# Performance work log

Hardware: AMD Instinct MI355X
Metric: run time of the kernel (lower is better)

Reference implementation:

```python
import jax, jax.numpy as jnp
import numpy as np


def setup_inputs() -> dict:
    key = jax.random.key(0)
    kq, kc = jax.random.split(key)
    query = jax.random.normal(kq, (64, 768), dtype=jnp.float32)
    corpus = jax.random.normal(kc, (500000, 768), dtype=jnp.float32)
    return {"query": query, "corpus": corpus, "k": 16}


def reference(query, corpus, k):
    # cosine similarity: (q @ c.T) / (|q|[:,None] * |c|[None,:])  -> [B, N]
    sim = jnp.einsum("bd,nd->bn", query, corpus)
    qn = jnp.linalg.norm(query, axis=1)   # [B]
    cn = jnp.linalg.norm(corpus, axis=1)  # [N]
    sim = sim / (qn[:, None] * cn[None, :])
    # top-k most similar corpus entries per query (largest=True)
    values, indices = jax.lax.top_k(sim, k)  # [B, k], [B, k]
    return values, indices
```

## Files before the change

### kernel.cpp

```cpp
#include <hip/hip_runtime.h>
#include <hip/hip_bf16.h>

#define D 768
#define NQ 64
#define TPB 256
#define GRID 1303
#define NWAVES (GRID * 4)
#define KSTEPS 24
#define SIMP 20
#define NS 8

typedef float    f32x4 __attribute__((ext_vector_type(4)));
typedef _Float16 h16x8 __attribute__((ext_vector_type(8)));

__device__ __forceinline__ bool kbetter(float v1, int i1, float v2, int i2) {
    return (v1 > v2) || (v1 == v2 && i1 < i2);
}

__device__ __forceinline__ void topk_insert(float (&tv)[16], int (&ti)[16], float v, int idx) {
    if (!kbetter(v, idx, tv[15], ti[15])) return;
    tv[15] = v; ti[15] = idx;
    #pragma unroll
    for (int s = 15; s >= 1; --s) {
        bool sw = kbetter(tv[s], ti[s], tv[s-1], ti[s-1]);
        float av = sw ? tv[s] : tv[s-1];
        float bv = sw ? tv[s-1] : tv[s];
        int   ai = sw ? ti[s] : ti[s-1];
        int   bi = sw ? ti[s-1] : ti[s];
        tv[s-1] = av; tv[s] = bv; ti[s-1] = ai; ti[s] = bi;
    }
}

__device__ __forceinline__ void bitonic16(float (&v)[16], int (&ix)[16]) {
    #pragma unroll
    for (int d = 8; d >= 1; d >>= 1) {
        #pragma unroll
        for (int i = 0; i < 16; ++i) {
            if ((i & d) == 0) {
                int j = i | d;
                bool sw = kbetter(v[j], ix[j], v[i], ix[i]);
                float av = sw ? v[j] : v[i];
                float bv = sw ? v[i] : v[j];
                int   ai = sw ? ix[j] : ix[i];
                int   bi = sw ? ix[i] : ix[j];
                v[i] = av; v[j] = bv; ix[i] = ai; ix[j] = bi;
            }
        }
    }
}

__device__ __forceinline__ void lane_merge(float (&v)[16], int (&ix)[16], int mask) {
    float pv[16]; int pix[16];
    #pragma unroll
    for (int i = 0; i < 16; ++i) {
        pv[i]  = __shfl_xor(v[15 - i], mask);
        pix[i] = __shfl_xor(ix[15 - i], mask);
    }
    #pragma unroll
    for (int i = 0; i < 16; ++i) {
        if (kbetter(pv[i], pix[i], v[i], ix[i])) { v[i] = pv[i]; ix[i] = pix[i]; }
    }
    bitonic16(v, ix);
}

__device__ __forceinline__ void sort64(float& v, int& ix, int l) {
    #pragma unroll
    for (int k = 2; k <= 64; k <<= 1) {
        #pragma unroll
        for (int j = k >> 1; j >= 1; j >>= 1) {
            float ov = __shfl_xor(v, j);
            int   oi = __shfl_xor(ix, j);
            bool dirDesc = ((l & k) == 0);
            bool lower   = ((l & j) == 0);
            bool takeBetter = (lower == dirDesc);
            bool ob = kbetter(ov, oi, v, ix);
            if (takeBetter == ob) { v = ov; ix = oi; }
        }
    }
}

__global__ __launch_bounds__(256)
void prep_kernel(const float* __restrict__ query, _Float16* __restrict__ qpk) {
    int b = blockIdx.x, t = threadIdx.x;
    const float* row = query + b * D;
    float vals[3]; float s = 0.f;
    #pragma unroll
    for (int j = 0; j < 3; ++j) { vals[j] = row[t + 256 * j]; s += vals[j] * vals[j]; }
    #pragma unroll
    for (int m = 1; m < 64; m <<= 1) s += __shfl_xor(s, m);
    __shared__ float ws4[4];
    if ((t & 63) == 0) ws4[t >> 6] = s;
    __syncthreads();
    float qn = sqrtf(ws4[0] + ws4[1] + ws4[2] + ws4[3]);
    int qf = b >> 4;
    #pragma unroll
    for (int j = 0; j < 3; ++j) {
        int col = t + 256 * j;
        float vn = vals[j] / qn;
        _Float16 h = (_Float16)vn;
        float r = vn - (float)h;
        _Float16 l2 = (_Float16)(r * 2048.0f);
        int ks = col >> 5, unit = (col >> 3) & 3, sub = col & 7;
        int lane = (b & 15) + unit * 16;
        size_t off = (((size_t)ks * 4 + qf) * 64 + lane) * 16 + sub;
        qpk[off]     = h;
        qpk[off + 8] = l2;
    }
}

__global__ __launch_bounds__(TPB, 2)
void sim_topk_kernel(const float* __restrict__ corpus,
                     const _Float16* __restrict__ qpk,
                     float2* __restrict__ cand,
                     int N, int NG) {
    __shared__ float scratch[4][NQ * SIMP];
    int t = threadIdx.x, w = t >> 6, l = t & 63;
    int ww = blockIdx.x * 4 + w;
    int n16 = l & 15, kg = l >> 4;
    float* sc = scratch[w];

    float tv[16]; int ti[16];
    #pragma unroll
    for (int s = 0; s < 16; ++s) { tv[s] = -INFINITY; ti[s] = 0x7fffffff; }

    for (int g = ww; g < NG; g += NWAVES) {
        long baseA = (long)g * 32;
        long rA = baseA + n16;      if (rA > N - 1) rA = N - 1;
        long rB = baseA + 16 + n16; if (rB > N - 1) rB = N - 1;
        const float* pA = corpus + (size_t)rA * D + kg * 8;
        const float* pB = corpus + (size_t)rB * D + kg * 8;

        f32x4 accAH[4], accAX[4], accBH[4], accBX[4];
        #pragma unroll
        for (int qf = 0; qf < 4; ++qf) {
            accAH[qf] = (f32x4)(0.f); accAX[qf] = (f32x4)(0.f);
            accBH[qf] = (f32x4)(0.f); accBX[qf] = (f32x4)(0.f);
        }
        float psA = 0.f, psB = 0.f;

        #pragma unroll 2
        for (int ks = 0; ks < KSTEPS; ++ks) {
            h16x8 qh[4], ql[4];
            #pragma unroll
            for (int qf = 0; qf < 4; ++qf) {
                const _Float16* qp = qpk + (((size_t)ks * 4 + qf) * 64 + l) * 16;
                qh[qf] = *(const h16x8*)qp;
                ql[qf] = *(const h16x8*)(qp + 8);
            }
            f32x4 a0 = *(const f32x4*)(pA + ks * 32);
            f32x4 a1 = *(const f32x4*)(pA + ks * 32 + 4);
            f32x4 b0 = *(const f32x4*)(pB + ks * 32);
            f32x4 b1 = *(const f32x4*)(pB + ks * 32 + 4);

            h16x8 hiA, loA, hiB, loB;
            #pragma unroll
            for (int i = 0; i < 4; ++i) {
                float va = a0[i]; _Float16 ha = (_Float16)va;
                hiA[i] = ha; loA[i] = (_Float16)((va - (float)ha) * 2048.0f);
                psA += va * va;
                float va1 = a1[i]; _Float16 ha1 = (_Float16)va1;
                hiA[4 + i] = ha1; loA[4 + i] = (_Float16)((va1 - (float)ha1) * 2048.0f);
                psA += va1 * va1;
                float vb = b0[i]; _Float16 hb = (_Float16)vb;
                hiB[i] = hb; loB[i] = (_Float16)((vb - (float)hb) * 2048.0f);
                psB += vb * vb;
                float vb1 = b1[i]; _Float16 hb1 = (_Float16)vb1;
                hiB[4 + i] = hb1; loB[4 + i] = (_Float16)((vb1 - (float)hb1) * 2048.0f);
                psB += vb1 * vb1;
            }
            #pragma unroll
            for (int qf = 0; qf < 4; ++qf) {
                accAH[qf] = __builtin_amdgcn_mfma_f32_16x16x32_f16(qh[qf], hiA, accAH[qf], 0, 0, 0);
                accAX[qf] = __builtin_amdgcn_mfma_f32_16x16x32_f16(qh[qf], loA, accAX[qf], 0, 0, 0);
                accAX[qf] = __builtin_amdgcn_mfma_f32_16x16x32_f16(ql[qf], hiA, accAX[qf], 0, 0, 0);
                accBH[qf] = __builtin_amdgcn_mfma_f32_16x16x32_f16(qh[qf], hiB, accBH[qf], 0, 0, 0);
                accBX[qf] = __builtin_amdgcn_mfma_f32_16x16x32_f16(qh[qf], loB, accBX[qf], 0, 0, 0);
                accBX[qf] = __builtin_amdgcn_mfma_f32_16x16x32_f16(ql[qf], hiB, accBX[qf], 0, 0, 0);
            }
        }

        psA += __shfl_xor(psA, 16); psA += __shfl_xor(psA, 32);
        psB += __shfl_xor(psB, 16); psB += __shfl_xor(psB, 32);
        float invA = 1.0f / sqrtf(psA);
        float invB = 1.0f / sqrtf(psB);

        #pragma unroll
        for (int qf = 0; qf < 4; ++qf)
            #pragma unroll
            for (int r = 0; r < 4; ++r) {
                int q = qf * 16 + kg * 4 + r;
                sc[q * SIMP + n16] = (accAH[qf][r] + accAX[qf][r] * (1.0f / 2048.0f)) * invA;
            }
        {
            f32x4 sv[4];
            #pragma unroll
            for (int j = 0; j < 4; ++j) sv[j] = *(const f32x4*)(sc + l * SIMP + j * 4);
            #pragma unroll
            for (int j = 0; j < 4; ++j)
                #pragma unroll
                for (int e = 0; e < 4; ++e) {
                    long gidx = baseA + j * 4 + e;
                    if (gidx < N) topk_insert(tv, ti, sv[j][e], (int)gidx);
                }
        }
        #pragma unroll
        for (int qf = 0; qf < 4; ++qf)
            #pragma unroll
            for (int r = 0; r < 4; ++r) {
                int q = qf * 16 + kg * 4 + r;
                sc[q * SIMP + n16] = (accBH[qf][r] + accBX[qf][r] * (1.0f / 2048.0f)) * invB;
            }
        {
            f32x4 sv[4];
            #pragma unroll
            for (int j = 0; j < 4; ++j) sv[j] = *(const f32x4*)(sc + l * SIMP + j * 4);
            #pragma unroll
            for (int j = 0; j < 4; ++j)
                #pragma unroll
                for (int e = 0; e < 4; ++e) {
                    long gidx = baseA + 16 + j * 4 + e;
                    if (gidx < N) topk_insert(tv, ti, sv[j][e], (int)gidx);
                }
        }
    }

    float2* dst = cand + ((size_t)l * NWAVES + ww) * 16;
    #pragma unroll
    for (int s = 0; s < 16; ++s) dst[s] = make_float2(tv[s], __int_as_float(ti[s]));
}

__global__ __launch_bounds__(256)
void merge1_kernel(const float2* __restrict__ cand, float2* __restrict__ cand2, int NWV) {
    int q = blockIdx.x >> 3, seg = blockIdx.x & (NS - 1);
    int t = threadIdx.x, w = t >> 6, l = t & 63;
    int total = NWV * 16;
    int chunk = (total + NS - 1) / NS;
    int e0 = seg * chunk, e1 = min(total, e0 + chunk);
    const float2* src = cand + (size_t)q * total;
    float tv[16]; int ti[16];
    #pragma unroll
    for (int s = 0; s < 16; ++s) { tv[s] = -INFINITY; ti[s] = 0x7fffffff; }
    for (int e = e0 + t; e < e1; e += 256) {
        float2 ce = src[e];
        topk_insert(tv, ti, ce.x, __float_as_int(ce.y));
    }
    lane_merge(tv, ti, 1);  lane_merge(tv, ti, 2);  lane_merge(tv, ti, 4);
    lane_merge(tv, ti, 8);  lane_merge(tv, ti, 16); lane_merge(tv, ti, 32);
    __shared__ float2 stage[64];
    if (l == 0) {
        #pragma unroll
        for (int s = 0; s < 16; ++s) stage[w * 16 + s] = make_float2(tv[s], __int_as_float(ti[s]));
    }
    __syncthreads();
    if (t < 64) {
        float2 ce = stage[t];
        float v = ce.x; int ix = __float_as_int(ce.y);
        sort64(v, ix, t);
        if (t < 16) cand2[((size_t)q * NS + seg) * 16 + t] = make_float2(v, __int_as_float(ix));
    }
}

__global__ __launch_bounds__(64)
void merge2_kernel(const float2* __restrict__ cand2, float* __restrict__ out) {
    int q = blockIdx.x, l = threadIdx.x;
    const float2* src = cand2 + (size_t)q * (NS * 16);
    float2 a = src[l], b = src[l + 64];
    float v1 = a.x; int i1 = __float_as_int(a.y);
    float v2 = b.x; int i2 = __float_as_int(b.y);
    sort64(v1, i1, l);
    sort64(v2, i2, l);
    float sv = __shfl(v2, (l - 16) & 63);
    int   si = __shfl(i2, (l - 16) & 63);
    float mv = (l < 16) ? v1 : ((l < 32) ? sv : -INFINITY);
    int   mi = (l < 16) ? i1 : ((l < 32) ? si : 0x7fffffff);
    sort64(mv, mi, l);
    if (l < 16) {
        out[q * 16 + l]           = mv;
        out[NQ * 16 + q * 16 + l] = (float)mi;
    }
}

extern "C" void kernel_launch(void* const* d_in, const int* in_sizes, int n_in,
                              void* d_out, int out_size, void* d_ws, size_t ws_size,
                              hipStream_t stream) {
    const float* query  = (const float*)d_in[0];
    const float* corpus = (const float*)d_in[1];
    int N  = in_sizes[1] / D;
    int NG = (N + 31) / 32;
    char* ws = (char*)d_ws;
    _Float16* qpk = (_Float16*)ws;
    float2*  cand = (float2*)(ws + 196608);
    size_t candBytes = (size_t)NQ * NWAVES * 16 * sizeof(float2);
    float2* cand2 = (float2*)(ws + 196608 + candBytes);
    float*   out  = (float*)d_out;

    prep_kernel<<<NQ, 256, 0, stream>>>(query, qpk);
    sim_topk_kernel<<<GRID, TPB, 0, stream>>>(corpus, qpk, cand, N, NG);
    merge1_kernel<<<NQ * NS, 256, 0, stream>>>(cand, cand2, NWAVES);
    merge2_kernel<<<NQ, 64, 0, stream>>>(cand2, out);
}
```

Before: 614.2 us.

## Split query and corpus rows across waves with software-pipelined loads

Each wave now computes 16 corpus rows against 32 queries, not 32 rows against all 64 queries, so the four waves of a block split a 32-row group by row half and query half. Accumulator registers drop sharply, launch bounds rise to 4 blocks per CU, and the k-loop is fully unrolled with double-buffered corpus and query loads for the next step. Lanes 0-31 and 32-63 hold separate top-k lists for the same query, so they are merged with lane_merge and only half the lanes write candidates. Fewer candidates go to the merge stage, but each corpus row is now converted and norm-summed by two waves, which duplicates that ALU and load work.

```diff
diff --git a/kernel.cpp b/kernel.cpp
--- a/kernel.cpp
+++ b/kernel.cpp
@@ -4,10 +4,10 @@
 #define D 768
 #define NQ 64
 #define TPB 256
-#define GRID 1303
-#define NWAVES (GRID * 4)
+#define GRID 1024
+#define NPAIR (GRID * 2)
 #define KSTEPS 24
-#define SIMP 20
+#define SCST 17
 #define NS 8
 
 typedef float    f32x4 __attribute__((ext_vector_type(4)));
@@ -108,14 +108,52 @@
     }
 }
 
-__global__ __launch_bounds__(TPB, 2)
+
+#define QLOADM(ks, qh0, ql0, qh1, ql1) do {                                    \
+    const _Float16* qp0 = qpk + (((size_t)(ks) * 4 + qb) * 64 + l) * 16;       \
+    qh0 = *(const h16x8*)qp0;  ql0 = *(const h16x8*)(qp0 + 8);                 \
+    const _Float16* qp1 = qp0 + 64 * 16;                                       \
+    qh1 = *(const h16x8*)qp1;  ql1 = *(const h16x8*)(qp1 + 8);                 \
+  } while (0)
+
+#define CLOADM(ks, c0, c1) do {                                                \
+    c0 = *(const f32x4*)(pc + (ks) * 32);                                      \
+    c1 = *(const f32x4*)(pc + (ks) * 32 + 4);                                  \
+  } while (0)
+
+#define STEPM(ks, c0, c1, qh0, ql0, qh1, ql1, n0, n1, nqh0, nql0, nqh1, nql1)  \
+  do {                                                                         \
+    if ((ks) + 1 < KSTEPS) {                                                   \
+        CLOADM((ks) + 1, n0, n1);                                              \
+        QLOADM((ks) + 1, nqh0, nql0, nqh1, nql1);                              \
+    }                                                                          \
+    h16x8 hi, lo;                                                              \
+    _Pragma("unroll")                                                          \
+    for (int i = 0; i < 4; ++i) {                                              \
+        float v0 = c0[i]; _Float16 h0 = (_Float16)v0;                          \
+        hi[i] = h0; lo[i] = (_Float16)((v0 - (float)h0) * 2048.0f);            \
+        ps += v0 * v0;                                                         \
+        float v1 = c1[i]; _Float16 h1 = (_Float16)v1;                          \
+        hi[4 + i] = h1; lo[4 + i] = (_Float16)((v1 - (float)h1) * 2048.0f);    \
+        ps += v1 * v1;                                                         \
+    }                                                                          \
+    aH0 = __builtin_amdgcn_mfma_f32_16x16x32_f16(qh0, hi, aH0, 0, 0, 0);       \
+    aX0 = __builtin_amdgcn_mfma_f32_16x16x32_f16(qh0, lo, aX0, 0, 0, 0);       \
+    aX0 = __builtin_amdgcn_mfma_f32_16x16x32_f16(ql0, hi, aX0, 0, 0, 0);       \
+    aH1 = __builtin_amdgcn_mfma_f32_16x16x32_f16(qh1, hi, aH1, 0, 0, 0);       \
+    aX1 = __builtin_amdgcn_mfma_f32_16x16x32_f16(qh1, lo, aX1, 0, 0, 0);       \
+    aX1 = __builtin_amdgcn_mfma_f32_16x16x32_f16(ql1, hi, aX1, 0, 0, 0);       \
+  } while (0)
+
+__global__ __launch_bounds__(TPB, 4)
 void sim_topk_kernel(const float* __restrict__ corpus,
                      const _Float16* __restrict__ qpk,
                      float2* __restrict__ cand,
                      int N, int NG) {
-    __shared__ float scratch[4][NQ * SIMP];
+    __shared__ float scratch[4][32 * SCST];
     int t = threadIdx.x, w = t >> 6, l = t & 63;
-    int ww = blockIdx.x * 4 + w;
+    int h  = w >> 1;
+    int qb = (w & 1) * 2;
     int n16 = l & 15, kg = l >> 4;
     float* sc = scratch[w];
 
@@ -123,110 +161,67 @@
     #pragma unroll
     for (int s = 0; s < 16; ++s) { tv[s] = -INFINITY; ti[s] = 0x7fffffff; }
 
-    for (int g = ww; g < NG; g += NWAVES) {
-        long baseA = (long)g * 32;
-        long rA = baseA + n16;      if (rA > N - 1) rA = N - 1;
-        long rB = baseA + 16 + n16; if (rB > N - 1) rB = N - 1;
-        const float* pA = corpus + (size_t)rA * D + kg * 8;
-        const float* pB = corpus + (size_t)rB * D + kg * 8;
-
-        f32x4 accAH[4], accAX[4], accBH[4], accBX[4];
-        #pragma unroll
-        for (int qf = 0; qf < 4; ++qf) {
-            accAH[qf] = (f32x4)(0.f); accAX[qf] = (f32x4)(0.f);
-            accBH[qf] = (f32x4)(0.f); accBX[qf] = (f32x4)(0.f);
-        }
-        float psA = 0.f, psB = 0.f;
-
-        #pragma unroll 2
-        for (int ks = 0; ks < KSTEPS; ++ks) {
-            h16x8 qh[4], ql[4];
-            #pragma unroll
-            for (int qf = 0; qf < 4; ++qf) {
-                const _Float16* qp = qpk + (((size_t)ks * 4 + qf) * 64 + l) * 16;
-                qh[qf] = *(const h16x8*)qp;
-                ql[qf] = *(const h16x8*)(qp + 8);
-            }
-            f32x4 a0 = *(const f32x4*)(pA + ks * 32);
-            f32x4 a1 = *(const f32x4*)(pA + ks * 32 + 4);
-            f32x4 b0 = *(const f32x4*)(pB + ks * 32);
-            f32x4 b1 = *(const f32x4*)(pB + ks * 32 + 4);
-
-            h16x8 hiA, loA, hiB, loB;
-            #pragma unroll
-            for (int i = 0; i < 4; ++i) {
-                float va = a0[i]; _Float16 ha = (_Float16)va;
-                hiA[i] = ha; loA[i] = (_Float16)((va - (float)ha) * 2048.0f);
-                psA += va * va;
-                float va1 = a1[i]; _Float16 ha1 = (_Float16)va1;
-                hiA[4 + i] = ha1; loA[4 + i] = (_Float16)((va1 - (float)ha1) * 2048.0f);
-                psA += va1 * va1;
-                float vb = b0[i]; _Float16 hb = (_Float16)vb;
-                hiB[i] = hb; loB[i] = (_Float16)((vb - (float)hb) * 2048.0f);
-                psB += vb * vb;
-                float vb1 = b1[i]; _Float16 hb1 = (_Float16)vb1;
-                hiB[4 + i] = hb1; loB[4 + i] = (_Float16)((vb1 - (float)hb1) * 2048.0f);
-                psB += vb1 * vb1;
-            }
-            #pragma unroll
-            for (int qf = 0; qf < 4; ++qf) {
-                accAH[qf] = __builtin_amdgcn_mfma_f32_16x16x32_f16(qh[qf], hiA, accAH[qf], 0, 0, 0);
-                accAX[qf] = __builtin_amdgcn_mfma_f32_16x16x32_f16(qh[qf], loA, accAX[qf], 0, 0, 0);
-                accAX[qf] = __builtin_amdgcn_mfma_f32_16x16x32_f16(ql[qf], hiA, accAX[qf], 0, 0, 0);
-                accBH[qf] = __builtin_amdgcn_mfma_f32_16x16x32_f16(qh[qf], hiB, accBH[qf], 0, 0, 0);
-                accBX[qf] = __builtin_amdgcn_mfma_f32_16x16x32_f16(qh[qf], loB, accBX[qf], 0, 0, 0);
-                accBX[qf] = __builtin_amdgcn_mfma_f32_16x16x32_f16(ql[qf], hiB, accBX[qf], 0, 0, 0);
-            }
-        }
-
-        psA += __shfl_xor(psA, 16); psA += __shfl_xor(psA, 32);
-        psB += __shfl_xor(psB, 16); psB += __shfl_xor(psB, 32);
-        float invA = 1.0f / sqrtf(psA);
-        float invB = 1.0f / sqrtf(psB);
-
-        #pragma unroll
-        for (int qf = 0; qf < 4; ++qf)
+    for (int g = blockIdx.x; g < NG; g += GRID) {
+        long rowg = (long)g * 32 + h * 16 + n16;
+        if (rowg > N - 1) rowg = N - 1;
+        const float* pc = corpus + (size_t)rowg * D + kg * 8;
+
+        f32x4 aH0 = (f32x4)(0.f), aX0 = (f32x4)(0.f);
+        f32x4 aH1 = (f32x4)(0.f), aX1 = (f32x4)(0.f);
+        float ps = 0.f;
+
+        f32x4 cA0, cA1, cB0, cB1;
+        h16x8 qhA0, qlA0, qhA1, qlA1, qhB0, qlB0, qhB1, qlB1;
+        CLOADM(0, cA0, cA1);
+        QLOADM(0, qhA0, qlA0, qhA1, qlA1);
+
+        #pragma unroll
+        for (int m = 0; m < KSTEPS / 2; ++m) {
+            STEPM(2 * m,     cA0, cA1, qhA0, qlA0, qhA1, qlA1,
+                             cB0, cB1, qhB0, qlB0, qhB1, qlB1);
+            STEPM(2 * m + 1, cB0, cB1, qhB0, qlB0, qhB1, qlB1,
+                             cA0, cA1, qhA0, qlA0, qhA1, qlA1);
+        }
+
+        ps += __shfl_xor(ps, 16);
+        ps += __shfl_xor(ps, 32);
+        float inv = 1.0f / sqrtf(ps);
+
+        #pragma unroll
+        for (int qf = 0; qf < 2; ++qf)
             #pragma unroll
             for (int r = 0; r < 4; ++r) {
-                int q = qf * 16 + kg * 4 + r;
-                sc[q * SIMP + n16] = (accAH[qf][r] + accAX[qf][r] * (1.0f / 2048.0f)) * invA;
+                int qloc = qf * 16 + kg * 4 + r;
+                float dH = qf ? aH1[r] : aH0[r];
+                float dX = qf ? aX1[r] : aX0[r];
+                sc[qloc * SCST + n16] = (dH + dX * (1.0f / 2048.0f)) * inv;
             }
         {
-            f32x4 sv[4];
+            int qloc = l & 31, nh = (l >> 5) * 8;
+            f32x4 s0 = *(const f32x4*)(sc + qloc * SCST + nh);
+            f32x4 s1 = *(const f32x4*)(sc + qloc * SCST + nh + 4);
+            long gbase = (long)g * 32 + h * 16 + nh;
             #pragma unroll
-            for (int j = 0; j < 4; ++j) sv[j] = *(const f32x4*)(sc + l * SIMP + j * 4);
+            for (int e = 0; e < 4; ++e) {
+                long gi = gbase + e;
+                if (gi < N) topk_insert(tv, ti, s0[e], (int)gi);
+            }
             #pragma unroll
-            for (int j = 0; j < 4; ++j)
-                #pragma unroll
-                for (int e = 0; e < 4; ++e) {
-                    long gidx = baseA + j * 4 + e;
-                    if (gidx < N) topk_insert(tv, ti, sv[j][e], (int)gidx);
-                }
-        }
-        #pragma unroll
-        for (int qf = 0; qf < 4; ++qf)
-            #pragma unroll
-            for (int r = 0; r < 4; ++r) {
-                int q = qf * 16 + kg * 4 + r;
-                sc[q * SIMP + n16] = (accBH[qf][r] + accBX[qf][r] * (1.0f / 2048.0f)) * invB;
-            }
-        {
-            f32x4 sv[4];
-            #pragma unroll
-            for (int j = 0; j < 4; ++j) sv[j] = *(const f32x4*)(sc + l * SIMP + j * 4);
-            #pragma unroll
-            for (int j = 0; j < 4; ++j)
-                #pragma unroll
-                for (int e = 0; e < 4; ++e) {
-                    long gidx = baseA + 16 + j * 4 + e;
-                    if (gidx < N) topk_insert(tv, ti, sv[j][e], (int)gidx);
-                }
-        }
-    }
-
-    float2* dst = cand + ((size_t)l * NWAVES + ww) * 16;
-    #pragma unroll
-    for (int s = 0; s < 16; ++s) dst[s] = make_float2(tv[s], __int_as_float(ti[s]));
+            for (int e = 0; e < 4; ++e) {
+                long gi = gbase + 4 + e;
+                if (gi < N) topk_insert(tv, ti, s1[e], (int)gi);
+            }
+        }
+    }
+
+    lane_merge(tv, ti, 32);
+    if (l < 32) {
+        int q = (w & 1) * 32 + l;
+        int pair = blockIdx.x * 2 + h;
+        float2* dst = cand + ((size_t)q * NPAIR + pair) * 16;
+        #pragma unroll
+        for (int s = 0; s < 16; ++s) dst[s] = make_float2(tv[s], __int_as_float(ti[s]));
+    }
 }
 
 __global__ __launch_bounds__(256)
@@ -290,12 +285,12 @@
     char* ws = (char*)d_ws;
     _Float16* qpk = (_Float16*)ws;
     float2*  cand = (float2*)(ws + 196608);
-    size_t candBytes = (size_t)NQ * NWAVES * 16 * sizeof(float2);
+    size_t candBytes = (size_t)NQ * NPAIR * 16 * sizeof(float2);
     float2* cand2 = (float2*)(ws + 196608 + candBytes);
     float*   out  = (float*)d_out;
 
     prep_kernel<<<NQ, 256, 0, stream>>>(query, qpk);
     sim_topk_kernel<<<GRID, TPB, 0, stream>>>(corpus, qpk, cand, N, NG);
-    merge1_kernel<<<NQ * NS, 256, 0, stream>>>(cand, cand2, NWAVES);
+    merge1_kernel<<<NQ * NS, 256, 0, stream>>>(cand, cand2, NPAIR);
     merge2_kernel<<<NQ, 64, 0, stream>>>(cand2, out);
 }
```

Result: slower. 1.564 ms (+154.6%).

## Split fused similarity+topk into separate sim kernel and streaming top-k merge kernel

Applied to the files above, without the earlier changes.

The fused kernel that computed similarities and kept per-lane top-k in registers is split in two. A leaner sim kernel (one 16-row tile per iteration, fewer registers, occupancy 4) writes the full similarity matrix to workspace with nontemporal stores. A new mergeA kernel streams that matrix and keeps the top-k. This frees MFMA waves from the branchy insertion work and raises occupancy, at the cost of writing and rereading a 128MB similarity buffer.

```diff
diff --git a/kernel.cpp b/kernel.cpp
--- a/kernel.cpp
+++ b/kernel.cpp
@@ -4,10 +4,11 @@
 #define D 768
 #define NQ 64
 #define TPB 256
-#define GRID 1303
-#define NWAVES (GRID * 4)
+#define GRID 1024
+#define NWT (GRID * 4)
 #define KSTEPS 24
-#define SIMP 20
+#define SCST 17
+#define NMW 4096
 #define NS 8
 
 typedef float    f32x4 __attribute__((ext_vector_type(4)));
@@ -108,123 +109,100 @@
     }
 }
 
-__global__ __launch_bounds__(TPB, 2)
-void sim_topk_kernel(const float* __restrict__ corpus,
-                     const _Float16* __restrict__ qpk,
-                     float2* __restrict__ cand,
-                     int N, int NG) {
-    __shared__ float scratch[4][NQ * SIMP];
+__global__ __launch_bounds__(TPB, 4)
+void sim_kernel(const float* __restrict__ corpus,
+                const _Float16* __restrict__ qpk,
+                float* __restrict__ simout, int N, int NG16) {
+    __shared__ float scratch[4][NQ * SCST];
     int t = threadIdx.x, w = t >> 6, l = t & 63;
     int ww = blockIdx.x * 4 + w;
     int n16 = l & 15, kg = l >> 4;
     float* sc = scratch[w];
 
-    float tv[16]; int ti[16];
-    #pragma unroll
-    for (int s = 0; s < 16; ++s) { tv[s] = -INFINITY; ti[s] = 0x7fffffff; }
-
-    for (int g = ww; g < NG; g += NWAVES) {
-        long baseA = (long)g * 32;
-        long rA = baseA + n16;      if (rA > N - 1) rA = N - 1;
-        long rB = baseA + 16 + n16; if (rB > N - 1) rB = N - 1;
-        const float* pA = corpus + (size_t)rA * D + kg * 8;
-        const float* pB = corpus + (size_t)rB * D + kg * 8;
-
-        f32x4 accAH[4], accAX[4], accBH[4], accBX[4];
-        #pragma unroll
-        for (int qf = 0; qf < 4; ++qf) {
-            accAH[qf] = (f32x4)(0.f); accAX[qf] = (f32x4)(0.f);
-            accBH[qf] = (f32x4)(0.f); accBX[qf] = (f32x4)(0.f);
-        }
-        float psA = 0.f, psB = 0.f;
+    for (int g = ww; g < NG16; g += NWT) {
+        long rowg = (long)g * 16 + n16;
+        if (rowg > N - 1) rowg = N - 1;
+        const float* pc = corpus + (size_t)rowg * D + kg * 8;
+
+        f32x4 accH[4], accX[4];
+        #pragma unroll
+        for (int qf = 0; qf < 4; ++qf) { accH[qf] = (f32x4)(0.f); accX[qf] = (f32x4)(0.f); }
+        float ps = 0.f;
 
         #pragma unroll 2
         for (int ks = 0; ks < KSTEPS; ++ks) {
-            h16x8 qh[4], ql[4];
+            f32x4 c0 = __builtin_nontemporal_load((const f32x4*)(pc + ks * 32));
+            f32x4 c1 = __builtin_nontemporal_load((const f32x4*)(pc + ks * 32 + 4));
+            h16x8 hi, lo;
+            #pragma unroll
+            for (int i = 0; i < 4; ++i) {
+                float v0 = c0[i]; _Float16 h0 = (_Float16)v0;
+                hi[i] = h0; lo[i] = (_Float16)((v0 - (float)h0) * 2048.0f);
+                ps += v0 * v0;
+                float v1 = c1[i]; _Float16 h1 = (_Float16)v1;
+                hi[4 + i] = h1; lo[4 + i] = (_Float16)((v1 - (float)h1) * 2048.0f);
+                ps += v1 * v1;
+            }
             #pragma unroll
             for (int qf = 0; qf < 4; ++qf) {
                 const _Float16* qp = qpk + (((size_t)ks * 4 + qf) * 64 + l) * 16;
-                qh[qf] = *(const h16x8*)qp;
-                ql[qf] = *(const h16x8*)(qp + 8);
-            }
-            f32x4 a0 = *(const f32x4*)(pA + ks * 32);
-            f32x4 a1 = *(const f32x4*)(pA + ks * 32 + 4);
-            f32x4 b0 = *(const f32x4*)(pB + ks * 32);
-            f32x4 b1 = *(const f32x4*)(pB + ks * 32 + 4);
-
-            h16x8 hiA, loA, hiB, loB;
-            #pragma unroll
-            for (int i = 0; i < 4; ++i) {
-                float va = a0[i]; _Float16 ha = (_Float16)va;
-                hiA[i] = ha; loA[i] = (_Float16)((va - (float)ha) * 2048.0f);
-                psA += va * va;
-                float va1 = a1[i]; _Float16 ha1 = (_Float16)va1;
-                hiA[4 + i] = ha1; loA[4 + i] = (_Float16)((va1 - (float)ha1) * 2048.0f);
-                psA += va1 * va1;
-                float vb = b0[i]; _Float16 hb = (_Float16)vb;
-                hiB[i] = hb; loB[i] = (_Float16)((vb - (float)hb) * 2048.0f);
-                psB += vb * vb;
-                float vb1 = b1[i]; _Float16 hb1 = (_Float16)vb1;
-                hiB[4 + i] = hb1; loB[4 + i] = (_Float16)((vb1 - (float)hb1) * 2048.0f);
-                psB += vb1 * vb1;
-            }
-            #pragma unroll
-            for (int qf = 0; qf < 4; ++qf) {
-                accAH[qf] = __builtin_amdgcn_mfma_f32_16x16x32_f16(qh[qf], hiA, accAH[qf], 0, 0, 0);
-                accAX[qf] = __builtin_amdgcn_mfma_f32_16x16x32_f16(qh[qf], loA, accAX[qf], 0, 0, 0);
-                accAX[qf] = __builtin_amdgcn_mfma_f32_16x16x32_f16(ql[qf], hiA, accAX[qf], 0, 0, 0);
-                accBH[qf] = __builtin_amdgcn_mfma_f32_16x16x32_f16(qh[qf], hiB, accBH[qf], 0, 0, 0);
-                accBX[qf] = __builtin_amdgcn_mfma_f32_16x16x32_f16(qh[qf], loB, accBX[qf], 0, 0, 0);
-                accBX[qf] = __builtin_amdgcn_mfma_f32_16x16x32_f16(ql[qf], hiB, accBX[qf], 0, 0, 0);
+                h16x8 qh = *(const h16x8*)qp;
+                h16x8 ql = *(const h16x8*)(qp + 8);
+                accH[qf] = __builtin_amdgcn_mfma_f32_16x16x32_f16(qh, hi, accH[qf], 0, 0, 0);
+                accX[qf] = __builtin_amdgcn_mfma_f32_16x16x32_f16(qh, lo, accX[qf], 0, 0, 0);
+                accX[qf] = __builtin_amdgcn_mfma_f32_16x16x32_f16(ql, hi, accX[qf], 0, 0, 0);
             }
         }
 
-        psA += __shfl_xor(psA, 16); psA += __shfl_xor(psA, 32);
-        psB += __shfl_xor(psB, 16); psB += __shfl_xor(psB, 32);
-        float invA = 1.0f / sqrtf(psA);
-        float invB = 1.0f / sqrtf(psB);
+        ps += __shfl_xor(ps, 16);
+        ps += __shfl_xor(ps, 32);
+        float inv = 1.0f / sqrtf(ps);
 
         #pragma unroll
         for (int qf = 0; qf < 4; ++qf)
             #pragma unroll
             for (int r = 0; r < 4; ++r) {
                 int q = qf * 16 + kg * 4 + r;
-                sc[q * SIMP + n16] = (accAH[qf][r] + accAX[qf][r] * (1.0f / 2048.0f)) * invA;
-            }
-        {
-            f32x4 sv[4];
-            #pragma unroll
-            for (int j = 0; j < 4; ++j) sv[j] = *(const f32x4*)(sc + l * SIMP + j * 4);
-            #pragma unroll
-            for (int j = 0; j < 4; ++j)
-                #pragma unroll
-                for (int e = 0; e < 4; ++e) {
-                    long gidx = baseA + j * 4 + e;
-                    if (gidx < N) topk_insert(tv, ti, sv[j][e], (int)gidx);
-                }
-        }
-        #pragma unroll
-        for (int qf = 0; qf < 4; ++qf)
-            #pragma unroll
-            for (int r = 0; r < 4; ++r) {
-                int q = qf * 16 + kg * 4 + r;
-                sc[q * SIMP + n16] = (accBH[qf][r] + accBX[qf][r] * (1.0f / 2048.0f)) * invB;
-            }
-        {
-            f32x4 sv[4];
-            #pragma unroll
-            for (int j = 0; j < 4; ++j) sv[j] = *(const f32x4*)(sc + l * SIMP + j * 4);
-            #pragma unroll
-            for (int j = 0; j < 4; ++j)
-                #pragma unroll
-                for (int e = 0; e < 4; ++e) {
-                    long gidx = baseA + 16 + j * 4 + e;
-                    if (gidx < N) topk_insert(tv, ti, sv[j][e], (int)gidx);
-                }
-        }
-    }
-
-    float2* dst = cand + ((size_t)l * NWAVES + ww) * 16;
+                sc[q * SCST + n16] = (accH[qf][r] + accX[qf][r] * (1.0f / 2048.0f)) * inv;
+            }
+        f32x4 sv[4];
+        #pragma unroll
+        for (int j4 = 0; j4 < 4; ++j4) sv[j4] = *(const f32x4*)(sc + l * SCST + j4 * 4);
+        float* so = simout + (size_t)g * 16 * NQ + l;
+        #pragma unroll
+        for (int j4 = 0; j4 < 4; ++j4)
+            #pragma unroll
+            for (int e = 0; e < 4; ++e)
+                __builtin_nontemporal_store(sv[j4][e], so + (size_t)(j4 * 4 + e) * NQ);
+    }
+}
+
+__global__ __launch_bounds__(256)
+void mergeA_kernel(const float* __restrict__ simout, float2* __restrict__ candA, int N) {
+    int t = threadIdx.x, w = t >> 6, l = t & 63;
+    int ww = blockIdx.x * 4 + w;
+    int chunk = (N + NMW - 1) / NMW;
+    int n0 = ww * chunk, n1 = min(N, n0 + chunk);
+
+    float tv[16]; int ti[16];
+    #pragma unroll
+    for (int s = 0; s < 16; ++s) { tv[s] = -INFINITY; ti[s] = 0x7fffffff; }
+
+    int n = n0;
+    for (; n + 8 <= n1; n += 8) {
+        float v[8];
+        #pragma unroll
+        for (int j = 0; j < 8; ++j)
+            v[j] = __builtin_nontemporal_load(simout + (size_t)(n + j) * NQ + l);
+        #pragma unroll
+        for (int j = 0; j < 8; ++j) topk_insert(tv, ti, v[j], n + j);
+    }
+    for (; n < n1; ++n) {
+        float v = __builtin_nontemporal_load(simout + (size_t)n * NQ + l);
+        topk_insert(tv, ti, v, n);
+    }
+
+    float2* dst = candA + ((size_t)l * NMW + ww) * 16;
     #pragma unroll
     for (int s = 0; s < 16; ++s) dst[s] = make_float2(tv[s], __int_as_float(ti[s]));
 }
@@ -285,17 +263,20 @@
                               hipStream_t stream) {
     const float* query  = (const float*)d_in[0];
     const float* corpus = (const float*)d_in[1];
-    int N  = in_sizes[1] / D;
-    int NG = (N + 31) / 32;
+    int N    = in_sizes[1] / D;
+    int NG16 = (N + 15) / 16;
     char* ws = (char*)d_ws;
-    _Float16* qpk = (_Float16*)ws;
-    float2*  cand = (float2*)(ws + 196608);
-    size_t candBytes = (size_t)NQ * NWAVES * 16 * sizeof(float2);
-    float2* cand2 = (float2*)(ws + 196608 + candBytes);
-    float*   out  = (float*)d_out;
+    _Float16* qpk  = (_Float16*)ws;
+    float* simout  = (float*)(ws + 196608);
+    size_t simBytes = (size_t)NG16 * 16 * NQ * sizeof(float);
+    float2* candA  = (float2*)(ws + 196608 + simBytes);
+    size_t candABytes = (size_t)NQ * NMW * 16 * sizeof(float2);
+    float2* cand2  = (float2*)(ws + 196608 + simBytes + candABytes);
+    float* out = (float*)d_out;
 
     prep_kernel<<<NQ, 256, 0, stream>>>(query, qpk);
-    sim_topk_kernel<<<GRID, TPB, 0, stream>>>(corpus, qpk, cand, N, NG);
-    merge1_kernel<<<NQ * NS, 256, 0, stream>>>(cand, cand2, NWAVES);
+    sim_kernel<<<GRID, TPB, 0, stream>>>(corpus, qpk, simout, N, NG16);
+    mergeA_kernel<<<NMW / 4, 256, 0, stream>>>(simout, candA, N);
+    merge1_kernel<<<NQ * NS, 256, 0, stream>>>(candA, cand2, NMW);
     merge2_kernel<<<NQ, 64, 0, stream>>>(cand2, out);
 }
```

After: 907.1 us. 47.7% more time.
